# Optimization experiments

Hardware: AMD Instinct MI355X
Metric: run time of the kernel (lower is better)

## Reference

```python
import jax, jax.numpy as jnp
import numpy as np

N = 100000        # nodes
E = 3200000       # edges (avg degree 32)
IN_F = 128
OUT_F = 64
ALPHA = 0.2       # LeakyReLU negative slope
EPS = 1e-5        # LayerNorm eps


def setup_inputs() -> dict:
    key = jax.random.key(0)
    k = jax.random.split(key, 5)
    x = jax.random.normal(k[0], (N, IN_F), jnp.float32)
    edge = jax.random.randint(k[1], (2, E), 0, N, dtype=jnp.int32)
    # kaiming-normal inits as in the torch module
    W = jax.random.normal(k[2], (OUT_F, IN_F), jnp.float32) * np.float32(np.sqrt(2.0 / IN_F))
    b = jnp.zeros((OUT_F,), jnp.float32)
    a = jax.random.normal(k[3], (2 * OUT_F,), jnp.float32) * np.float32(np.sqrt(2.0 / (2 * OUT_F)))
    gamma = jnp.ones((OUT_F,), jnp.float32)
    beta = jnp.zeros((OUT_F,), jnp.float32)
    return {"x": x, "edge": edge, "W": W, "b": b, "a": a, "gamma": gamma, "beta": beta}


def reference(x, edge, W, b, a, gamma, beta):
    # h = Linear(in->out)
    h = x @ W.T + b                                   # [N, OUT_F]
    src, dst = edge[0], edge[1]
    # edge score a · cat(h[src], h[dst]) == (h @ a_l)[src] + (h @ a_r)[dst]
    sl = h @ a[:OUT_F]                                # [N]
    sr = h @ a[OUT_F:]                                # [N]
    score = sl[src] + sr[dst]                         # [E]
    lrelu = jnp.where(score > 0, score, ALPHA * score)
    edge_e = jnp.exp(-lrelu)                          # [E] (dropout=0 / eval)
    # sparse spmm: h_prime[i] = sum_{e: src_e==i} edge_e * h[dst_e]
    msg = edge_e[:, None] * h[dst]                    # [E, OUT_F]
    h_prime = jax.ops.segment_sum(msg, src, num_segments=N)  # [N, OUT_F]
    # LayerNorm over feature dim (biased variance, as torch)
    mu = jnp.mean(h_prime, axis=-1, keepdims=True)
    var = jnp.mean(jnp.square(h_prime - mu), axis=-1, keepdims=True)
    h_norm = (h_prime - mu) * jax.lax.rsqrt(var + EPS) * gamma + beta
    # concat=True -> ELU
    return jax.nn.elu(h_norm)
```

## Files before the change

kernel.cpp:

```cpp
#include <hip/hip_runtime.h>
#include <hip/hip_fp16.h>
#include <cstdint>
#include <cstddef>

#define INF_  128
#define OUTF  64
#define ALPHA 0.2f
#define LN_EPS 1e-5f

#define PBLK  1024
#define NP2   784
#define NPS   1024
#define TILE  3584
#define LOC2  128
#define CSRCAP 4608
#define MAXK  9

typedef __attribute__((ext_vector_type(8))) _Float16 half8;
typedef __attribute__((ext_vector_type(4))) float    f32x4;

__global__ __launch_bounds__(256) void gemm_kernel(
    const float* __restrict__ x, const float* __restrict__ W,
    const float* __restrict__ b, const float* __restrict__ a,
    __half* __restrict__ hh, float* __restrict__ sl, float* __restrict__ sr, int n)
{
    __shared__ half8 wfrag_lds[16][64];

    const int tid  = threadIdx.x;
    const int lane = tid & 63;
    const int wv   = tid >> 6;
    const int col  = lane & 15;
    const int quad = lane >> 4;

    for (int idx = tid; idx < 1024; idx += 256) {
        const int l  = idx & 63, ct = idx >> 6;
        const int c  = ct >> 2,  t  = ct & 3;
        const int row = 4 * (l & 15) + t;
        const int k0  = 32 * c + 8 * (l >> 4);
        const float4 f0 = ((const float4*)W)[row * 32 + (k0 >> 2)];
        const float4 f1 = ((const float4*)W)[row * 32 + (k0 >> 2) + 1];
        half8 h;
        h[0] = (_Float16)f0.x; h[1] = (_Float16)f0.y;
        h[2] = (_Float16)f0.z; h[3] = (_Float16)f0.w;
        h[4] = (_Float16)f1.x; h[5] = (_Float16)f1.y;
        h[6] = (_Float16)f1.z; h[7] = (_Float16)f1.w;
        wfrag_lds[ct][l] = h;
    }
    __syncthreads();

    half8 bf[4][4];
    #pragma unroll
    for (int c = 0; c < 4; c++)
        #pragma unroll
        for (int t = 0; t < 4; t++)
            bf[c][t] = wfrag_lds[c * 4 + t][lane];

    const float4 b4  = ((const float4*)b)[col];
    const float4 al4 = ((const float4*)a)[col];
    const float4 ar4 = ((const float4*)a)[16 + col];

    const int ntile  = (n + 15) >> 4;
    const int wgid   = blockIdx.x * 4 + wv;
    const int nwaves = gridDim.x * 4;

    for (int tile = wgid; tile < ntile; tile += nwaves) {
        const int node0 = tile << 4;
        const int xr    = min(node0 + col, n - 1);
        const float* xrow = x + (size_t)xr * INF_ + 8 * quad;

        f32x4 acc0 = {0,0,0,0}, acc1 = {0,0,0,0}, acc2 = {0,0,0,0}, acc3 = {0,0,0,0};
        #pragma unroll
        for (int c = 0; c < 4; c++) {
            const float4 f0 = *(const float4*)(xrow + 32 * c);
            const float4 f1 = *(const float4*)(xrow + 32 * c + 4);
            half8 af;
            af[0] = (_Float16)f0.x; af[1] = (_Float16)f0.y;
            af[2] = (_Float16)f0.z; af[3] = (_Float16)f0.w;
            af[4] = (_Float16)f1.x; af[5] = (_Float16)f1.y;
            af[6] = (_Float16)f1.z; af[7] = (_Float16)f1.w;
            acc0 = __builtin_amdgcn_mfma_f32_16x16x32_f16(af, bf[c][0], acc0, 0, 0, 0);
            acc1 = __builtin_amdgcn_mfma_f32_16x16x32_f16(af, bf[c][1], acc1, 0, 0, 0);
            acc2 = __builtin_amdgcn_mfma_f32_16x16x32_f16(af, bf[c][2], acc2, 0, 0, 0);
            acc3 = __builtin_amdgcn_mfma_f32_16x16x32_f16(af, bf[c][3], acc3, 0, 0, 0);
        }

        #pragma unroll
        for (int reg = 0; reg < 4; reg++) {
            const int node = node0 + quad * 4 + reg;
            const float v0 = acc0[reg] + b4.x;
            const float v1 = acc1[reg] + b4.y;
            const float v2 = acc2[reg] + b4.z;
            const float v3 = acc3[reg] + b4.w;
            float p = v0 * al4.x + v1 * al4.y + v2 * al4.z + v3 * al4.w;
            float q = v0 * ar4.x + v1 * ar4.y + v2 * ar4.z + v3 * ar4.w;
            p += __shfl_xor(p, 1); p += __shfl_xor(p, 2);
            p += __shfl_xor(p, 4); p += __shfl_xor(p, 8);
            q += __shfl_xor(q, 1); q += __shfl_xor(q, 2);
            q += __shfl_xor(q, 4); q += __shfl_xor(q, 8);
            if (node < n) {
                ushort4 u;
                u.x = __half_as_ushort(__float2half(v0));
                u.y = __half_as_ushort(__float2half(v1));
                u.z = __half_as_ushort(__float2half(v2));
                u.w = __half_as_ushort(__float2half(v3));
                ((ushort4*)hh)[(size_t)node * 16 + col] = u;
                if (col == 0) { sl[node] = p; sr[node] = q; }
            }
        }
    }
}

__global__ __launch_bounds__(512) void count_kernel(
    const int* __restrict__ src, int* __restrict__ M, int E)
{
    __shared__ int hist[NPS];
    const int t = threadIdx.x;
    const int b = blockIdx.x;
    for (int i = t; i < NPS; i += 512) hist[i] = 0;
    __syncthreads();
    const int chunk = (E + PBLK - 1) / PBLK;
    const int lo = b * chunk;
    const int hi = min(E, lo + chunk);
    for (int e = lo + t; e < hi; e += 512)
        atomicAdd(&hist[src[e] >> 7], 1);
    __syncthreads();
    for (int p = t; p < NP2; p += 512)
        M[(size_t)p * PBLK + b] = hist[p];
}

__global__ __launch_bounds__(1024) void rowscan_kernel(
    int* __restrict__ M, int* __restrict__ rowsum)
{
    __shared__ int ws[16];
    const int p    = blockIdx.x;
    const int t    = threadIdx.x;
    const int lane = t & 63;
    const int wv   = t >> 6;
    const int v = M[(size_t)p * PBLK + t];
    int s = v;
    #pragma unroll
    for (int d = 1; d < 64; d <<= 1) {
        const int u = __shfl(s, lane - d);
        if (lane >= d) s += u;
    }
    if (lane == 63) ws[wv] = s;
    __syncthreads();
    int cross = 0;
    #pragma unroll
    for (int w = 0; w < 16; w++)
        if (w < wv) cross += ws[w];
    M[(size_t)p * PBLK + t] = cross + s - v;
    if (t == PBLK - 1) rowsum[p] = cross + s;
}

__global__ __launch_bounds__(1024) void pbase_kernel(
    const int* __restrict__ rowsum, int* __restrict__ pbase)
{
    __shared__ int part[NPS];
    const int t = threadIdx.x;
    const int v = (t < NP2) ? rowsum[t] : 0;
    part[t] = v;
    __syncthreads();
    for (int d = 1; d < NPS; d <<= 1) {
        const int u = (t >= d) ? part[t - d] : 0;
        __syncthreads();
        part[t] += u;
        __syncthreads();
    }
    if (t < NP2) pbase[t] = part[t] - v;
    if (t == NP2 - 1) pbase[NP2] = part[t];
}

__global__ __launch_bounds__(512) void part_scatter(
    const int* __restrict__ src, const int* __restrict__ dst,
    const int* __restrict__ M, const int* __restrict__ pbase,
    int* __restrict__ pk, int E)
{
    __shared__ int hist[NPS];
    __shared__ int bnd[NPS + 1];
    __shared__ int cur[NPS];
    __shared__ int gbase[NP2];
    __shared__ int buf[TILE];
    __shared__ unsigned char pbuf[TILE];
    __shared__ int csum[16];
    __shared__ int csb[16];

    const int t    = threadIdx.x;
    const int b    = blockIdx.x;
    const int lane = t & 63;
    const int wv   = t >> 6;

    for (int p = t; p < NP2; p += 512)
        gbase[p] = pbase[p] + M[(size_t)p * PBLK + b];

    const int chunk = (E + PBLK - 1) / PBLK;
    const int lo = b * chunk;
    const int hi = min(E, lo + chunk);

    for (int tb = lo; tb < hi; tb += TILE) {
        const int tcnt = min(TILE, hi - tb);
        for (int i = t; i < NPS; i += 512) hist[i] = 0;
        __syncthreads();

        int pp[7], pay[7];
        #pragma unroll
        for (int k = 0; k < 7; k++) {
            const int e = tb + t + k * 512;
            pp[k] = -1;
            if (e < hi) {
                const int s = src[e];
                pp[k]  = s >> 7;
                pay[k] = ((s & 127) << 17) | dst[e];
                atomicAdd(&hist[pp[k]], 1);
            }
        }
        __syncthreads();

        int vA = hist[wv * 64 + lane];
        int vB = hist[(wv + 8) * 64 + lane];
        int sA = vA, sB = vB;
        #pragma unroll
        for (int d = 1; d < 64; d <<= 1) {
            const int uA = __shfl(sA, lane - d);
            const int uB = __shfl(sB, lane - d);
            if (lane >= d) { sA += uA; sB += uB; }
        }
        if (lane == 63) { csum[wv] = sA; csum[wv + 8] = sB; }
        __syncthreads();
        if (t == 0) {
            int r = 0;
            #pragma unroll
            for (int c2 = 0; c2 < 16; c2++) { csb[c2] = r; r += csum[c2]; }
            bnd[NPS] = r;
        }
        __syncthreads();
        {
            const int eA = csb[wv] + sA - vA;
            const int eB = csb[wv + 8] + sB - vB;
            bnd[wv * 64 + lane]       = eA;
            bnd[(wv + 8) * 64 + lane] = eB;
            cur[wv * 64 + lane]       = eA;
            cur[(wv + 8) * 64 + lane] = eB;
        }
        __syncthreads();

        #pragma unroll
        for (int k = 0; k < 7; k++) {
            if (pp[k] >= 0) {
                const int r = atomicAdd(&cur[pp[k]], 1);
                buf[r]  = pay[k];
                pbuf[r] = (unsigned char)(pp[k] & 255);
            }
        }
        __syncthreads();

        const int c1 = bnd[256], c2_ = bnd[512], c3 = bnd[768];
        for (int idx = t; idx < tcnt; idx += 512) {
            const int phi = (idx >= c1) + (idx >= c2_) + (idx >= c3);
            const int p   = (phi << 8) | (int)pbuf[idx];
            pk[gbase[p] + (idx - bnd[p])] = buf[idx];
        }
        __syncthreads();

        for (int p = t; p < NP2; p += 512) gbase[p] += bnd[p + 1] - bnd[p];
        __syncthreads();
    }
}

__global__ __launch_bounds__(512) void gat_fused(
    const int* __restrict__ pk, const int* __restrict__ pbase,
    const float* __restrict__ sl, const float* __restrict__ sr,
    const __half* __restrict__ hh,
    const float* __restrict__ gamma, const float* __restrict__ beta,
    float* __restrict__ out, int n)
{
    __shared__ int    ldst[CSRCAP];
    __shared__ __half lwgt[CSRCAP];
    __shared__ float  lsl[LOC2];
    __shared__ int    lhist[LOC2];
    __shared__ int    lbase[LOC2 + 1];
    __shared__ int    wtot_;

    const int B     = blockIdx.x;
    const int t     = threadIdx.x;
    const int lane  = t & 63;
    const int wv    = t >> 6;
    const int fgrp  = lane & 15;
    const int equad = lane >> 4;

    if (t < LOC2) {
        lhist[t] = 0;
        const int g = (B << 7) + t;
        lsl[t] = (g < n) ? sl[g] : 0.f;
    }
    const int p0  = pbase[B];
    const int cnt = min(pbase[B + 1] - p0, CSRCAP);
    __syncthreads();

    const int myn = (cnt > t) ? (cnt - t + 511) >> 9 : 0;
    int   pkr[MAXK];
    float wf[MAXK];
    int   rk[MAXK];
    #pragma unroll
    for (int k = 0; k < MAXK; k++) {
        if (k < myn) {
            const int v = pk[p0 + t + (k << 9)];
            pkr[k] = v;
            const int s = (v >> 17) & 127;
            rk[k] = atomicAdd(&lhist[s], 1);
            const float sc = lsl[s] + sr[v & 0x1FFFF];
            const float lr = sc > 0.f ? sc : ALPHA * sc;
            wf[k] = __expf(-lr);
        }
    }
    __syncthreads();

    int sv = 0, vv = 0;
    if (t < 128) {
        vv = lhist[t]; sv = vv;
        #pragma unroll
        for (int d = 1; d < 64; d <<= 1) {
            const int u = __shfl(sv, lane - d);
            if (lane >= d) sv += u;
        }
        if (t == 63) wtot_ = sv;
    }
    __syncthreads();
    if (t < 128) {
        const int base = (t >= 64) ? wtot_ : 0;
        lbase[t] = base + sv - vv;
        if (t == 127) lbase[128] = base + sv;
    }
    __syncthreads();

    #pragma unroll
    for (int k = 0; k < MAXK; k++) {
        if (k < myn) {
            const int v = pkr[k];
            const int s = (v >> 17) & 127;
            const int p = lbase[s] + rk[k];
            ldst[p] = v & 0x1FFFF;
            lwgt[p] = __float2half(wf[k]);
        }
    }
    __syncthreads();

    const float4 gm4 = ((const float4*)gamma)[fgrp];
    const float4 bt4 = ((const float4*)beta)[fgrp];

    for (int k = wv; k < LOC2; k += 8) {
        const int node = (B << 7) + k;
        const int nb   = lbase[k];
        const int len  = lbase[k + 1] - nb;

        float4 acc = make_float4(0.f, 0.f, 0.f, 0.f);

        const int e0 = equad, e1 = 4 + equad;
        int dA = 0, dB = 0; float wA = 0.f, wB = 0.f;
        if (e0 < len) { dA = ldst[nb + e0]; wA = __half2float(lwgt[nb + e0]); }
        if (e1 < len) { dB = ldst[nb + e1]; wB = __half2float(lwgt[nb + e1]); }
        uint2 uA = ((const uint2*)hh)[(size_t)dA * 16 + fgrp];
        uint2 uB = ((const uint2*)hh)[(size_t)dB * 16 + fgrp];

        for (int tt = 0; tt < len; tt += 8) {
            uint2 nA = make_uint2(0u, 0u), nB = make_uint2(0u, 0u);
            float nwA = 0.f, nwB = 0.f;
            if (tt + 8 < len) {
                const int f0 = tt + 8 + equad, f1 = tt + 12 + equad;
                int xA = 0, xB = 0;
                if (f0 < len) { xA = ldst[nb + f0]; nwA = __half2float(lwgt[nb + f0]); }
                if (f1 < len) { xB = ldst[nb + f1]; nwB = __half2float(lwgt[nb + f1]); }
                nA = ((const uint2*)hh)[(size_t)xA * 16 + fgrp];
                nB = ((const uint2*)hh)[(size_t)xB * 16 + fgrp];
            }
            const float2 fA0 = __half22float2(*(const __half2*)&uA.x);
            const float2 fA1 = __half22float2(*(const __half2*)&uA.y);
            const float2 fB0 = __half22float2(*(const __half2*)&uB.x);
            const float2 fB1 = __half22float2(*(const __half2*)&uB.y);
            acc.x = fmaf(wA, fA0.x, acc.x); acc.y = fmaf(wA, fA0.y, acc.y);
            acc.z = fmaf(wA, fA1.x, acc.z); acc.w = fmaf(wA, fA1.y, acc.w);
            acc.x = fmaf(wB, fB0.x, acc.x); acc.y = fmaf(wB, fB0.y, acc.y);
            acc.z = fmaf(wB, fB1.x, acc.z); acc.w = fmaf(wB, fB1.y, acc.w);
            uA = nA; uB = nB; wA = nwA; wB = nwB;
        }

        acc.x += __shfl_xor(acc.x, 16); acc.x += __shfl_xor(acc.x, 32);
        acc.y += __shfl_xor(acc.y, 16); acc.y += __shfl_xor(acc.y, 32);
        acc.z += __shfl_xor(acc.z, 16); acc.z += __shfl_xor(acc.z, 32);
        acc.w += __shfl_xor(acc.w, 16); acc.w += __shfl_xor(acc.w, 32);

        float s1 = acc.x + acc.y + acc.z + acc.w;
        float s2 = acc.x * acc.x + acc.y * acc.y + acc.z * acc.z + acc.w * acc.w;
        #pragma unroll
        for (int dd = 1; dd < 16; dd <<= 1) {
            s1 += __shfl_xor(s1, dd);
            s2 += __shfl_xor(s2, dd);
        }
        const float mu  = s1 * (1.f / 64.f);
        const float var = fmaxf(s2 * (1.f / 64.f) - mu * mu, 0.f);
        const float rs  = rsqrtf(var + LN_EPS);

        float4 y;
        y.x = (acc.x - mu) * rs * gm4.x + bt4.x;
        y.y = (acc.y - mu) * rs * gm4.y + bt4.y;
        y.z = (acc.z - mu) * rs * gm4.z + bt4.z;
        y.w = (acc.w - mu) * rs * gm4.w + bt4.w;
        y.x = y.x > 0.f ? y.x : __expf(y.x) - 1.f;
        y.y = y.y > 0.f ? y.y : __expf(y.y) - 1.f;
        y.z = y.z > 0.f ? y.z : __expf(y.z) - 1.f;
        y.w = y.w > 0.f ? y.w : __expf(y.w) - 1.f;
        if (node < n && equad == 0)
            ((float4*)out)[(size_t)node * 16 + fgrp] = y;
    }
}

extern "C" void kernel_launch(void* const* d_in, const int* in_sizes, int n_in,
                              void* d_out, int out_size, void* d_ws, size_t ws_size,
                              hipStream_t stream)
{
    const float* x     = (const float*)d_in[0];
    const int*   edge  = (const int*)  d_in[1];
    const float* W     = (const float*)d_in[2];
    const float* b     = (const float*)d_in[3];
    const float* a     = (const float*)d_in[4];
    const float* gamma = (const float*)d_in[5];
    const float* beta  = (const float*)d_in[6];
    float* out = (float*)d_out;

    const int n = in_sizes[0] / INF_;
    const int E = in_sizes[1] / 2;
    const int* src = edge;
    const int* dst = edge + E;
    const int npart = (n + LOC2 - 1) >> 7;

    char* ws = (char*)d_ws;
    size_t offb = 0;
    auto alloc = [&](size_t bytes) -> void* {
        void* p = ws + offb;
        offb = (offb + bytes + 255) & ~(size_t)255;
        return p;
    };
    __half* hh     = (__half*)alloc((size_t)n * OUTF * 2);
    float*  sl     = (float*) alloc((size_t)n * 4);
    float*  sr     = (float*) alloc((size_t)n * 4);
    int*    M      = (int*)   alloc((size_t)NP2 * PBLK * 4);
    int*    rowsum = (int*)   alloc((size_t)NP2 * 4);
    int*    pbase  = (int*)   alloc((size_t)(NP2 + 1) * 4);
    int*    pk     = (int*)   alloc((size_t)E * 4);

    hipLaunchKernelGGL(count_kernel,   dim3(PBLK),  dim3(512),  0, stream, src, M, E);
    hipLaunchKernelGGL(rowscan_kernel, dim3(NP2),   dim3(1024), 0, stream, M, rowsum);
    hipLaunchKernelGGL(pbase_kernel,   dim3(1),     dim3(1024), 0, stream, rowsum, pbase);
    hipLaunchKernelGGL(gemm_kernel,    dim3(1024),  dim3(256),  0, stream, x, W, b, a, hh, sl, sr, n);
    hipLaunchKernelGGL(part_scatter,   dim3(PBLK),  dim3(512),  0, stream, src, dst, M, pbase, pk, E);
    hipLaunchKernelGGL(gat_fused,      dim3(npart), dim3(512),  0, stream, pk, pbase, sl, sr, hh, gamma, beta, out, n);
}
```

Before: 250.4 us.

## Split each node partition across two blocks and widen scatter blocks

The partition scatter now uses 256 blocks of 1024 threads with larger tiles, and the per-block scans are simplified to match. The fused GAT kernel launches two blocks per 128-node partition. Each block reads the whole partition's edge list but keeps only the edges for its 64 nodes, which halves the per-block LDS footprint and doubles the grid for more occupancy. The cost is reading and filtering each partition's packed edges twice, plus new HCAP clamps that could silently drop edges if one half holds more than 3072 of them.

After: 235.8 us. 1.06x faster.

```diff
diff --git a/kernel.cpp b/kernel.cpp
--- a/kernel.cpp
+++ b/kernel.cpp
@@ -8,12 +8,12 @@
 #define ALPHA 0.2f
 #define LN_EPS 1e-5f
 
-#define PBLK  1024
+#define PBLK  256
 #define NP2   784
 #define NPS   1024
-#define TILE  3584
-#define LOC2  128
-#define CSRCAP 4608
+#define TILE  8192
+#define HCAP  3072
+#define PCNTMAX 4608
 #define MAXK  9
 
 typedef __attribute__((ext_vector_type(8))) _Float16 half8;
@@ -128,10 +128,10 @@
         M[(size_t)p * PBLK + b] = hist[p];
 }
 
-__global__ __launch_bounds__(1024) void rowscan_kernel(
+__global__ __launch_bounds__(256) void rowscan_kernel(
     int* __restrict__ M, int* __restrict__ rowsum)
 {
-    __shared__ int ws[16];
+    __shared__ int ws[4];
     const int p    = blockIdx.x;
     const int t    = threadIdx.x;
     const int lane = t & 63;
@@ -147,7 +147,7 @@
     __syncthreads();
     int cross = 0;
     #pragma unroll
-    for (int w = 0; w < 16; w++)
+    for (int w = 0; w < 4; w++)
         if (w < wv) cross += ws[w];
     M[(size_t)p * PBLK + t] = cross + s - v;
     if (t == PBLK - 1) rowsum[p] = cross + s;
@@ -171,7 +171,7 @@
     if (t == NP2 - 1) pbase[NP2] = part[t];
 }
 
-__global__ __launch_bounds__(512) void part_scatter(
+__global__ __launch_bounds__(1024) void part_scatter(
     const int* __restrict__ src, const int* __restrict__ dst,
     const int* __restrict__ M, const int* __restrict__ pbase,
     int* __restrict__ pk, int E)
@@ -182,15 +182,15 @@
     __shared__ int gbase[NP2];
     __shared__ int buf[TILE];
     __shared__ unsigned char pbuf[TILE];
-    __shared__ int csum[16];
-    __shared__ int csb[16];
+    __shared__ int wsum[16];
+    __shared__ int wbase[16];
 
     const int t    = threadIdx.x;
     const int b    = blockIdx.x;
     const int lane = t & 63;
     const int wv   = t >> 6;
 
-    for (int p = t; p < NP2; p += 512)
+    for (int p = t; p < NP2; p += 1024)
         gbase[p] = pbase[p] + M[(size_t)p * PBLK + b];
 
     const int chunk = (E + PBLK - 1) / PBLK;
@@ -199,13 +199,13 @@
 
     for (int tb = lo; tb < hi; tb += TILE) {
         const int tcnt = min(TILE, hi - tb);
-        for (int i = t; i < NPS; i += 512) hist[i] = 0;
-        __syncthreads();
-
-        int pp[7], pay[7];
-        #pragma unroll
-        for (int k = 0; k < 7; k++) {
-            const int e = tb + t + k * 512;
+        hist[t] = 0;
+        __syncthreads();
+
+        int pp[8], pay[8];
+        #pragma unroll
+        for (int k = 0; k < 8; k++) {
+            const int e = tb + t + k * 1024;
             pp[k] = -1;
             if (e < hi) {
                 const int s = src[e];
@@ -216,36 +216,36 @@
         }
         __syncthreads();
 
-        int vA = hist[wv * 64 + lane];
-        int vB = hist[(wv + 8) * 64 + lane];
-        int sA = vA, sB = vB;
+        const int v = hist[t];
+        int s = v;
         #pragma unroll
         for (int d = 1; d < 64; d <<= 1) {
-            const int uA = __shfl(sA, lane - d);
-            const int uB = __shfl(sB, lane - d);
-            if (lane >= d) { sA += uA; sB += uB; }
-        }
-        if (lane == 63) { csum[wv] = sA; csum[wv + 8] = sB; }
-        __syncthreads();
-        if (t == 0) {
-            int r = 0;
+            const int u = __shfl(s, lane - d);
+            if (lane >= d) s += u;
+        }
+        if (lane == 63) wsum[wv] = s;
+        __syncthreads();
+        if (t < 16) {
+            const int xv = wsum[t];
+            int sc = xv;
             #pragma unroll
-            for (int c2 = 0; c2 < 16; c2++) { csb[c2] = r; r += csum[c2]; }
-            bnd[NPS] = r;
+            for (int d = 1; d < 16; d <<= 1) {
+                const int u = __shfl(sc, t - d);
+                if (t >= d) sc += u;
+            }
+            wbase[t] = sc - xv;
         }
         __syncthreads();
         {
-            const int eA = csb[wv] + sA - vA;
-            const int eB = csb[wv + 8] + sB - vB;
-            bnd[wv * 64 + lane]       = eA;
-            bnd[(wv + 8) * 64 + lane] = eB;
-            cur[wv * 64 + lane]       = eA;
-            cur[(wv + 8) * 64 + lane] = eB;
-        }
-        __syncthreads();
-
-        #pragma unroll
-        for (int k = 0; k < 7; k++) {
+            const int eb = wbase[wv] + s - v;
+            bnd[t] = eb;
+            cur[t] = eb;
+            if (t == 1023) bnd[1024] = eb + v;
+        }
+        __syncthreads();
+
+        #pragma unroll
+        for (int k = 0; k < 8; k++) {
             if (pp[k] >= 0) {
                 const int r = atomicAdd(&cur[pp[k]], 1);
                 buf[r]  = pay[k];
@@ -255,14 +255,14 @@
         __syncthreads();
 
         const int c1 = bnd[256], c2_ = bnd[512], c3 = bnd[768];
-        for (int idx = t; idx < tcnt; idx += 512) {
+        for (int idx = t; idx < tcnt; idx += 1024) {
             const int phi = (idx >= c1) + (idx >= c2_) + (idx >= c3);
             const int p   = (phi << 8) | (int)pbuf[idx];
             pk[gbase[p] + (idx - bnd[p])] = buf[idx];
         }
         __syncthreads();
 
-        for (int p = t; p < NP2; p += 512) gbase[p] += bnd[p + 1] - bnd[p];
+        for (int p = t; p < NP2; p += 1024) gbase[p] += bnd[p + 1] - bnd[p];
         __syncthreads();
     }
 }
@@ -274,27 +274,28 @@
     const float* __restrict__ gamma, const float* __restrict__ beta,
     float* __restrict__ out, int n)
 {
-    __shared__ int    ldst[CSRCAP];
-    __shared__ __half lwgt[CSRCAP];
-    __shared__ float  lsl[LOC2];
-    __shared__ int    lhist[LOC2];
-    __shared__ int    lbase[LOC2 + 1];
-    __shared__ int    wtot_;
-
-    const int B     = blockIdx.x;
+    __shared__ int    ldst[HCAP];
+    __shared__ __half lwgt[HCAP];
+    __shared__ float  lsl[64];
+    __shared__ int    lhist[64];
+    __shared__ int    lbase[65];
+
+    const int Bh    = blockIdx.x;
+    const int P     = Bh >> 1;
+    const int hb    = Bh & 1;
     const int t     = threadIdx.x;
     const int lane  = t & 63;
     const int wv    = t >> 6;
     const int fgrp  = lane & 15;
     const int equad = lane >> 4;
 
-    if (t < LOC2) {
+    if (t < 64) {
         lhist[t] = 0;
-        const int g = (B << 7) + t;
+        const int g = (P << 7) + (hb << 6) + t;
         lsl[t] = (g < n) ? sl[g] : 0.f;
     }
-    const int p0  = pbase[B];
-    const int cnt = min(pbase[B + 1] - p0, CSRCAP);
+    const int p0  = pbase[P];
+    const int cnt = min(pbase[P + 1] - p0, PCNTMAX);
     __syncthreads();
 
     const int myn = (cnt > t) ? (cnt - t + 511) >> 9 : 0;
@@ -303,44 +304,45 @@
     int   rk[MAXK];
     #pragma unroll
     for (int k = 0; k < MAXK; k++) {
+        rk[k] = -1;
         if (k < myn) {
-            const int v = pk[p0 + t + (k << 9)];
-            pkr[k] = v;
-            const int s = (v >> 17) & 127;
-            rk[k] = atomicAdd(&lhist[s], 1);
-            const float sc = lsl[s] + sr[v & 0x1FFFF];
-            const float lr = sc > 0.f ? sc : ALPHA * sc;
-            wf[k] = __expf(-lr);
-        }
-    }
-    __syncthreads();
-
-    int sv = 0, vv = 0;
-    if (t < 128) {
-        vv = lhist[t]; sv = vv;
+            const int v  = pk[p0 + t + (k << 9)];
+            const int s7 = (v >> 17) & 127;
+            if ((s7 >> 6) == hb) {
+                pkr[k] = v;
+                const int s6 = s7 & 63;
+                rk[k] = atomicAdd(&lhist[s6], 1);
+                const float sc = lsl[s6] + sr[v & 0x1FFFF];
+                const float lr = sc > 0.f ? sc : ALPHA * sc;
+                wf[k] = __expf(-lr);
+            }
+        }
+    }
+    __syncthreads();
+
+    if (wv == 0) {
+        const int v = lhist[lane];
+        int s = v;
         #pragma unroll
         for (int d = 1; d < 64; d <<= 1) {
-            const int u = __shfl(sv, lane - d);
-            if (lane >= d) sv += u;
-        }
-        if (t == 63) wtot_ = sv;
-    }
-    __syncthreads();
-    if (t < 128) {
-        const int base = (t >= 64) ? wtot_ : 0;
-        lbase[t] = base + sv - vv;
-        if (t == 127) lbase[128] = base + sv;
+            const int u = __shfl(s, lane - d);
+            if (lane >= d) s += u;
+        }
+        lbase[lane] = s - v;
+        if (lane == 63) lbase[64] = s;
     }
     __syncthreads();
 
     #pragma unroll
     for (int k = 0; k < MAXK; k++) {
-        if (k < myn) {
+        if (rk[k] >= 0) {
             const int v = pkr[k];
-            const int s = (v >> 17) & 127;
-            const int p = lbase[s] + rk[k];
-            ldst[p] = v & 0x1FFFF;
-            lwgt[p] = __float2half(wf[k]);
+            const int s6 = (v >> 17) & 63;
+            const int p  = lbase[s6] + rk[k];
+            if (p < HCAP) {
+                ldst[p] = v & 0x1FFFF;
+                lwgt[p] = __float2half(wf[k]);
+            }
         }
     }
     __syncthreads();
@@ -348,10 +350,11 @@
     const float4 gm4 = ((const float4*)gamma)[fgrp];
     const float4 bt4 = ((const float4*)beta)[fgrp];
 
-    for (int k = wv; k < LOC2; k += 8) {
-        const int node = (B << 7) + k;
-        const int nb   = lbase[k];
-        const int len  = lbase[k + 1] - nb;
+    for (int k = wv; k < 64; k += 8) {
+        const int node = (P << 7) + (hb << 6) + k;
+        const int nb   = min(lbase[k], HCAP);
+        const int ne   = min(lbase[k + 1], HCAP);
+        const int len  = ne - nb;
 
         float4 acc = make_float4(0.f, 0.f, 0.f, 0.f);
 
@@ -431,7 +434,8 @@
     const int E = in_sizes[1] / 2;
     const int* src = edge;
     const int* dst = edge + E;
-    const int npart = (n + LOC2 - 1) >> 7;
+    const int npart = (n + 127) >> 7;
+    const int nhalf = npart * 2;
 
     char* ws = (char*)d_ws;
     size_t offb = 0;
@@ -449,9 +453,9 @@
     int*    pk     = (int*)   alloc((size_t)E * 4);
 
     hipLaunchKernelGGL(count_kernel,   dim3(PBLK),  dim3(512),  0, stream, src, M, E);
-    hipLaunchKernelGGL(rowscan_kernel, dim3(NP2),   dim3(1024), 0, stream, M, rowsum);
+    hipLaunchKernelGGL(rowscan_kernel, dim3(NP2),   dim3(256),  0, stream, M, rowsum);
     hipLaunchKernelGGL(pbase_kernel,   dim3(1),     dim3(1024), 0, stream, rowsum, pbase);
     hipLaunchKernelGGL(gemm_kernel,    dim3(1024),  dim3(256),  0, stream, x, W, b, a, hh, sl, sr, n);
-    hipLaunchKernelGGL(part_scatter,   dim3(PBLK),  dim3(512),  0, stream, src, dst, M, pbase, pk, E);
-    hipLaunchKernelGGL(gat_fused,      dim3(npart), dim3(512),  0, stream, pk, pbase, sl, sr, hh, gamma, beta, out, n);
-}
+    hipLaunchKernelGGL(part_scatter,   dim3(PBLK),  dim3(1024), 0, stream, src, dst, M, pbase, pk, E);
+    hipLaunchKernelGGL(gat_fused,      dim3(nhalf), dim3(512),  0, stream, pk, pbase, sl, sr, hh, gamma, beta, out, n);
+}
```
